# Kernel optimization log

Hardware: AMD Instinct MI355X
Metric: run time of the kernel (lower is better)

The kernel has to match this reference:

```python
import jax, jax.numpy as jnp
import numpy as np

N = 100000
E = 3200000
IN_CH, HID, OUT = 256, 64, 32


def setup_inputs() -> dict:
    key = jax.random.key(0)
    ks = jax.random.split(key, 8)
    x = jax.random.normal(ks[0], (N, IN_CH), dtype=jnp.float32)
    edge_index = jax.random.randint(ks[1], (2, E), 0, N, dtype=jnp.int64)
    # Glorot-ish init for weights, zeros for biases (PyG GCNConv: lin has no bias; conv bias added post-aggregation)
    W1 = jax.random.normal(ks[2], (IN_CH, HID), dtype=jnp.float32) / np.sqrt(IN_CH)
    b1 = jnp.zeros((HID,), dtype=jnp.float32)
    W2 = jax.random.normal(ks[3], (HID, OUT), dtype=jnp.float32) / np.sqrt(HID)
    b2 = jnp.zeros((OUT,), dtype=jnp.float32)
    Wc = jax.random.normal(ks[4], (OUT, 1), dtype=jnp.float32) / np.sqrt(OUT)
    bc = jnp.zeros((1,), dtype=jnp.float32)
    return {"x": x, "edge_index": edge_index, "W1": W1, "b1": b1,
            "W2": W2, "b2": b2, "Wc": Wc, "bc": bc}


def _gcn_norm(edge_index, num_nodes):
    # Add self-loops (PyG default), compute symmetric normalization D^{-1/2} A D^{-1/2}
    loops = jnp.arange(num_nodes, dtype=edge_index.dtype)
    row = jnp.concatenate([edge_index[0], loops])  # source
    col = jnp.concatenate([edge_index[1], loops])  # target (aggregation index)
    ones = jnp.ones(row.shape[0], dtype=jnp.float32)
    deg = jax.ops.segment_sum(ones, col, num_segments=num_nodes)
    dis = jnp.where(deg > 0, jax.lax.rsqrt(jnp.maximum(deg, 1e-12)), 0.0)
    norm = dis[row] * dis[col]  # [E+N]
    return row, col, norm


def _gcn_conv(x, W, b, row, col, norm, num_nodes):
    h = x @ W                                   # [N, F_out] dense transform first
    msg = h[row] * norm[:, None]                # gather + scale per edge
    agg = jax.ops.segment_sum(msg, col, num_segments=num_nodes)
    return agg + b


def reference(x, edge_index, W1, b1, W2, b2, Wc, bc):
    num_nodes = x.shape[0]
    row, col, norm = _gcn_norm(edge_index, num_nodes)
    h = jax.nn.elu(_gcn_conv(x, W1, b1, row, col, norm, num_nodes))
    h = jax.nn.elu(_gcn_conv(h, W2, b2, row, col, norm, num_nodes))
    return (h @ Wc + bc)[:, 0]                  # squeeze(1) -> [N]
```

## Files before the change

### kernel.cpp

```cpp
#include <hip/hip_runtime.h>
#include <hip/hip_fp16.h>
#include <math.h>

#define N_NODES 100000
#define N_EDGES 3200000
#define IN_CH   256
#define HID     64
#define OUTC    32
#define NB      ((N_NODES + 255) / 256)
#define NBUCK   ((N_NODES + 127) / 128)
#define CHUNK   4096
#define EPT     16
#define CAP     4608

static constexpr size_t align256(size_t x) { return (x + 255) & ~(size_t)255; }
static constexpr size_t OFF_DEG  = 0;
static constexpr size_t OFF_PTR  = OFF_DEG  + align256((size_t)N_NODES * 4);
static constexpr size_t OFF_BSUM = OFF_PTR  + align256((size_t)N_NODES * 4);
static constexpr size_t OFF_GCUR = OFF_BSUM + align256(512 * 4);
static constexpr size_t OFF_DIS  = OFF_GCUR + align256((size_t)NBUCK * 4);
static constexpr size_t OFF_SRC  = OFF_DIS  + align256((size_t)N_NODES * 4);
static constexpr size_t OFF_PART = OFF_SRC  + align256((size_t)N_EDGES * 4);
static constexpr size_t OFF_S1   = OFF_PART;
static constexpr size_t OFF_S2   = OFF_PART + align256((size_t)NBUCK * CAP * 4);

__global__ __launch_bounds__(256) void bucket_init(int* __restrict__ gcur) {
    int b = blockIdx.x * 256 + threadIdx.x;
    if (b < NBUCK) gcur[b] = b * CAP;
}

__global__ __launch_bounds__(256) void partition_edges(const int* __restrict__ row,
                                                       const int* __restrict__ col,
                                                       int* __restrict__ gcur,
                                                       int* __restrict__ part) {
    __shared__ int lhist[NBUCK];
    __shared__ int lbase[NBUCK];
    const int t  = threadIdx.x;
    const int e0 = blockIdx.x * CHUNK;
    for (int i = t; i < NBUCK; i += 256) lhist[i] = 0;
    __syncthreads();

    int pk[EPT], br[EPT];
#pragma unroll
    for (int i = 0; i < EPT; ++i) {
        int e = e0 + i * 256 + t;
        if (e < N_EDGES) {
            int d = col[e];
            int b = d >> 7;
            int r = atomicAdd(&lhist[b], 1);
            pk[i] = row[e] | ((d & 127) << 17);
            br[i] = b | (r << 10);
        } else {
            br[i] = -1;
        }
    }
    __syncthreads();

    const int off = (int)((blockIdx.x * 131u) % NBUCK);
    for (int i = t; i < NBUCK; i += 256) {
        int bb = i + off;
        if (bb >= NBUCK) bb -= NBUCK;
        int c = lhist[bb];
        lbase[bb] = (c > 0) ? atomicAdd(&gcur[bb], c) : 0;
    }
    __syncthreads();

#pragma unroll
    for (int i = 0; i < EPT; ++i) {
        if (br[i] >= 0) {
            int b = br[i] & 1023;
            int r = br[i] >> 10;
            part[lbase[b] + r] = pk[i];
        }
    }
}

__global__ __launch_bounds__(256) void bucket_hist(const int* __restrict__ gcur,
                                                   const int* __restrict__ part,
                                                   int* __restrict__ deg,
                                                   float* __restrict__ dis) {
    __shared__ int lh[128];
    const int b = blockIdx.x;
    const int t = threadIdx.x;
    if (t < 128) lh[t] = 0;
    __syncthreads();
    const int cnt = gcur[b] - b * CAP;
    for (int i = t; i < cnt; i += 256)
        atomicAdd(&lh[part[(size_t)b * CAP + i] >> 17], 1);
    __syncthreads();
    int v = b * 128 + t;
    if (t < 128 && v < N_NODES) {
        int d = lh[t];
        deg[v] = d;
        dis[v] = rsqrtf((float)d + 1.0f);
    }
}

__global__ __launch_bounds__(256) void scan_block_sums(const int* __restrict__ deg,
                                                       int* __restrict__ bsum) {
    __shared__ int buf[256];
    unsigned i = blockIdx.x * 256u + threadIdx.x;
    int v = (i < N_NODES) ? deg[i] : 0;
    buf[threadIdx.x] = v;
    __syncthreads();
    for (int off = 128; off > 0; off >>= 1) {
        if (threadIdx.x < (unsigned)off) buf[threadIdx.x] += buf[threadIdx.x + off];
        __syncthreads();
    }
    if (threadIdx.x == 0) bsum[blockIdx.x] = buf[0];
}

__global__ __launch_bounds__(512) void scan_bsum(int* __restrict__ bsum) {
    __shared__ int buf[512];
    int t = threadIdx.x;
    int v = (t < NB) ? bsum[t] : 0;
    buf[t] = v;
    __syncthreads();
    for (int off = 1; off < 512; off <<= 1) {
        int add = (t >= off) ? buf[t - off] : 0;
        __syncthreads();
        buf[t] += add;
        __syncthreads();
    }
    if (t < NB) bsum[t] = buf[t] - v;
}

__global__ __launch_bounds__(256) void scan_block_scan(const int* __restrict__ deg,
                                                       const int* __restrict__ bsum,
                                                       int* __restrict__ ptr) {
    __shared__ int buf[256];
    unsigned i = blockIdx.x * 256u + threadIdx.x;
    int v = (i < N_NODES) ? deg[i] : 0;
    buf[threadIdx.x] = v;
    __syncthreads();
    for (int off = 1; off < 256; off <<= 1) {
        int add = (threadIdx.x >= (unsigned)off) ? buf[threadIdx.x - off] : 0;
        __syncthreads();
        buf[threadIdx.x] += add;
        __syncthreads();
    }
    if (i < N_NODES) ptr[i] = bsum[blockIdx.x] + buf[threadIdx.x] - v;
}

__global__ __launch_bounds__(256) void bucket_fill(const int* __restrict__ gcur,
                                                   const int* __restrict__ part,
                                                   const int* __restrict__ ptr,
                                                   int* __restrict__ srcs) {
    __shared__ int lcur[128];
    const int b = blockIdx.x;
    const int t = threadIdx.x;
    if (t < 128) lcur[t] = 0;
    __syncthreads();
    const int cnt = gcur[b] - b * CAP;
    for (int i = t; i < cnt; i += 256) {
        int p    = part[(size_t)b * CAP + i];
        int dlow = p >> 17;
        int src  = p & 0x1FFFF;
        int r    = atomicAdd(&lcur[dlow], 1);
        srcs[ptr[b * 128 + dlow] + r] = src;
    }
}

__global__ __launch_bounds__(256) void gemm1(const float* __restrict__ x,
                                             const float* __restrict__ W1,
                                             const float* __restrict__ dis,
                                             __half* __restrict__ s1h) {
    __shared__ float wlds[64 * HID];
    __shared__ float xlds[64 * 68];

    const int t  = threadIdx.x;
    const int tx = t & 15;
    const int ty = t >> 4;
    const int row0 = blockIdx.x * 64;

    float acc[4][4] = {{0.f}};

    for (int kt = 0; kt < IN_CH / 64; ++kt) {
        {
            const float4* w4 = (const float4*)(W1 + (size_t)kt * 64 * HID);
            float4* l4 = (float4*)wlds;
#pragma unroll
            for (int i = 0; i < 4; ++i) l4[i * 256 + t] = w4[i * 256 + t];
        }
        {
#pragma unroll
            for (int i = 0; i < 4; ++i) {
                int L  = i * 256 + t;
                int rl = L >> 4;
                int k4 = L & 15;
                int rg = row0 + rl;
                float4 v;
                if (rg < N_NODES) v = ((const float4*)x)[(size_t)rg * 64 + kt * 16 + k4];
                else              v = make_float4(0.f, 0.f, 0.f, 0.f);
                *(float4*)(&xlds[rl * 68 + k4 * 4]) = v;
            }
        }
        __syncthreads();

        const float4* wl4 = (const float4*)wlds;
#pragma unroll 4
        for (int k4 = 0; k4 < 16; ++k4) {
            float4 xv[4];
#pragma unroll
            for (int i = 0; i < 4; ++i)
                xv[i] = *(const float4*)(&xlds[(ty * 4 + i) * 68 + k4 * 4]);
#pragma unroll
            for (int kk = 0; kk < 4; ++kk) {
                float4 bv = wl4[(k4 * 4 + kk) * 16 + tx];
#pragma unroll
                for (int i = 0; i < 4; ++i) {
                    const float* xf = (const float*)&xv[i];
                    float a = xf[kk];
                    acc[i][0] += a * bv.x;
                    acc[i][1] += a * bv.y;
                    acc[i][2] += a * bv.z;
                    acc[i][3] += a * bv.w;
                }
            }
        }
        __syncthreads();
    }

#pragma unroll
    for (int i = 0; i < 4; ++i) {
        int rr = row0 + ty * 4 + i;
        if (rr < N_NODES) {
            float d = dis[rr];
            __half2 p0 = __floats2half2_rn(acc[i][0] * d, acc[i][1] * d);
            __half2 p1 = __floats2half2_rn(acc[i][2] * d, acc[i][3] * d);
            __half2* dst = (__half2*)(s1h + (size_t)rr * HID + tx * 4);
            dst[0] = p0;
            dst[1] = p1;
        }
    }
}

__global__ __launch_bounds__(256) void gather1(const __half* __restrict__ s1h,
                                               const int* __restrict__ ptr,
                                               const int* __restrict__ srcs,
                                               const float* __restrict__ dis,
                                               const float* __restrict__ b1,
                                               const float* __restrict__ W2,
                                               __half* __restrict__ s2h) {
    __shared__ float w2lds[HID * OUTC];
    __shared__ float hbuf[4][HID];

    const int t = threadIdx.x;
    {
        float4* l4 = (float4*)w2lds;
        const float4* s4 = (const float4*)W2;
        l4[t] = s4[t];
        l4[256 + t] = s4[256 + t];
    }
    __syncthreads();

    const int j = t & 63;
    const int w = t >> 6;
    const int l = j & 31;
    const int h = j >> 5;
    const int v = __builtin_amdgcn_readfirstlane(blockIdx.x * 4 + w);
    const __half2* s12 = (const __half2*)s1h;

    float2 acc;
    {
        float2 self = __half22float2(s12[(size_t)v * 32 + l]);
        acc = (h == 0) ? self : make_float2(0.f, 0.f);
    }
    const int beg = ptr[v];
    const int end = (v + 1 < N_NODES) ? ptr[v + 1] : N_EDGES;
    int k = beg;
    for (; k + 8 <= end; k += 8) {
        int u0 = srcs[k],     u1 = srcs[k + 1], u2 = srcs[k + 2], u3 = srcs[k + 3];
        int u4 = srcs[k + 4], u5 = srcs[k + 5], u6 = srcs[k + 6], u7 = srcs[k + 7];
        int a0 = (h == 0) ? u0 : u1;
        int a1 = (h == 0) ? u2 : u3;
        int a2 = (h == 0) ? u4 : u5;
        int a3 = (h == 0) ? u6 : u7;
        float2 g0 = __half22float2(s12[(size_t)a0 * 32 + l]);
        float2 g1 = __half22float2(s12[(size_t)a1 * 32 + l]);
        float2 g2 = __half22float2(s12[(size_t)a2 * 32 + l]);
        float2 g3 = __half22float2(s12[(size_t)a3 * 32 + l]);
        acc.x += (g0.x + g1.x) + (g2.x + g3.x);
        acc.y += (g0.y + g1.y) + (g2.y + g3.y);
    }
    for (; k + 2 <= end; k += 2) {
        int u0 = srcs[k], u1 = srcs[k + 1];
        int a = (h == 0) ? u0 : u1;
        float2 g = __half22float2(s12[(size_t)a * 32 + l]);
        acc.x += g.x;
        acc.y += g.y;
    }
    if (k < end && h == 0) {
        float2 g = __half22float2(s12[(size_t)srcs[k] * 32 + l]);
        acc.x += g.x;
        acc.y += g.y;
    }
    acc.x += __shfl_xor(acc.x, 32, 64);
    acc.y += __shfl_xor(acc.y, 32, 64);

    float dv = dis[v];
    float2 bb = *(const float2*)(b1 + 2 * l);
    float t0 = dv * acc.x + bb.x;
    float t1 = dv * acc.y + bb.y;
    float h0 = t0 > 0.f ? t0 : (expf(t0) - 1.f);
    float h1 = t1 > 0.f ? t1 : (expf(t1) - 1.f);
    if (h == 0) {
        hbuf[w][2 * l]     = h0;
        hbuf[w][2 * l + 1] = h1;
    }

    const int jo = j & 31;
    const int kb = (j >> 5) * 32;
    float p = 0.f;
#pragma unroll
    for (int kk = 0; kk < 32; ++kk)
        p += hbuf[w][kb + kk] * w2lds[(kb + kk) * OUTC + jo];
    p += __shfl_xor(p, 32, 64);
    if (j < 32) {
        s2h[(size_t)v * OUTC + jo] = __float2half(dv * p);
    }
}

__global__ __launch_bounds__(256) void gather2(const __half* __restrict__ s2h,
                                               const int* __restrict__ ptr,
                                               const int* __restrict__ srcs,
                                               const float* __restrict__ dis,
                                               const float* __restrict__ b2,
                                               const float* __restrict__ Wc,
                                               const float* __restrict__ bc,
                                               float* __restrict__ out) {
    const int j = threadIdx.x & 63;
    const int w = threadIdx.x >> 6;
    const int l = j & 15;
    const int q = j >> 4;
    const int v = __builtin_amdgcn_readfirstlane(blockIdx.x * 4 + w);
    const __half2* s22 = (const __half2*)s2h;

    float2 acc;
    {
        float2 self = __half22float2(s22[(size_t)v * 16 + l]);
        acc = (q == 0) ? self : make_float2(0.f, 0.f);
    }
    const int beg = ptr[v];
    const int end = (v + 1 < N_NODES) ? ptr[v + 1] : N_EDGES;
    int k = beg;
    for (; k + 8 <= end; k += 8) {
        int a0 = srcs[k + q];
        int a1 = srcs[k + 4 + q];
        float2 g0 = __half22float2(s22[(size_t)a0 * 16 + l]);
        float2 g1 = __half22float2(s22[(size_t)a1 * 16 + l]);
        acc.x += g0.x + g1.x;
        acc.y += g0.y + g1.y;
    }
    for (; k + 4 <= end; k += 4) {
        int a = srcs[k + q];
        float2 g = __half22float2(s22[(size_t)a * 16 + l]);
        acc.x += g.x;
        acc.y += g.y;
    }
    int rem = end - k;
    if (q < rem) {
        int a = srcs[k + q];
        float2 g = __half22float2(s22[(size_t)a * 16 + l]);
        acc.x += g.x;
        acc.y += g.y;
    }
    acc.x += __shfl_xor(acc.x, 16, 64);
    acc.x += __shfl_xor(acc.x, 32, 64);
    acc.y += __shfl_xor(acc.y, 16, 64);
    acc.y += __shfl_xor(acc.y, 32, 64);

    float dv = dis[v];
    float2 bb = *(const float2*)(b2 + 2 * l);
    float t0 = dv * acc.x + bb.x;
    float t1 = dv * acc.y + bb.y;
    float h0 = t0 > 0.f ? t0 : (expf(t0) - 1.f);
    float h1 = t1 > 0.f ? t1 : (expf(t1) - 1.f);
    float2 wc = *(const float2*)(Wc + 2 * l);
    float p = h0 * wc.x + h1 * wc.y;
#pragma unroll
    for (int off = 8; off > 0; off >>= 1) p += __shfl_xor(p, off, 64);
    if (j == 0) out[v] = p + bc[0];
}

extern "C" void kernel_launch(void* const* d_in, const int* in_sizes, int n_in,
                              void* d_out, int out_size, void* d_ws, size_t ws_size,
                              hipStream_t stream) {
    const float* x  = (const float*)d_in[0];
    const int*   ei = (const int*)d_in[1];
    const float* W1 = (const float*)d_in[2];
    const float* b1 = (const float*)d_in[3];
    const float* W2 = (const float*)d_in[4];
    const float* b2 = (const float*)d_in[5];
    const float* Wc = (const float*)d_in[6];
    const float* bc = (const float*)d_in[7];
    float* out = (float*)d_out;

    const int* row = ei;
    const int* col = ei + N_EDGES;

    char* ws = (char*)d_ws;
    int*    deg  = (int*)   (ws + OFF_DEG);
    int*    ptr  = (int*)   (ws + OFF_PTR);
    int*    bsum = (int*)   (ws + OFF_BSUM);
    int*    gcur = (int*)   (ws + OFF_GCUR);
    float*  dis  = (float*) (ws + OFF_DIS);
    int*    srcs = (int*)   (ws + OFF_SRC);
    int*    part = (int*)   (ws + OFF_PART);
    __half* s1h  = (__half*)(ws + OFF_S1);
    __half* s2h  = (__half*)(ws + OFF_S2);

    bucket_init    <<<(NBUCK + 255) / 256, 256, 0, stream>>>(gcur);
    partition_edges<<<(N_EDGES + CHUNK - 1) / CHUNK, 256, 0, stream>>>(row, col, gcur, part);
    bucket_hist    <<<NBUCK, 256, 0, stream>>>(gcur, part, deg, dis);
    scan_block_sums<<<NB, 256, 0, stream>>>(deg, bsum);
    scan_bsum      <<<1, 512, 0, stream>>>(bsum);
    scan_block_scan<<<NB, 256, 0, stream>>>(deg, bsum, ptr);
    bucket_fill    <<<NBUCK, 256, 0, stream>>>(gcur, part, ptr, srcs);

    gemm1  <<<(N_NODES + 63) / 64, 256, 0, stream>>>(x, W1, dis, s1h);
    gather1<<<N_NODES / 4, 256, 0, stream>>>(s1h, ptr, srcs, dis, b1, W2, s2h);
    gather2<<<N_NODES / 4, 256, 0, stream>>>(s2h, ptr, srcs, dis, b2, Wc, bc, out);
}
```

Measured before the change: 417.6 us.

## Replace global degree scan with per-bucket local CSR offsets and deepen gather unroll

Builds the CSR with begin/end pointers local to each bucket's fixed-capacity region, computed by an in-block prefix scan inside bucket_hist. This removes the three global scan kernels and their launches. The source array becomes padded to NBUCK*CAP entries, and bucket_fill caches its base offsets in LDS. The gather loops are also unrolled to 16 edges per iteration, which puts more loads in flight at the cost of more registers.

Measured after the change: 414.5 us. About the same (-0.7%).

```diff
diff --git a/kernel.cpp b/kernel.cpp
--- a/kernel.cpp
+++ b/kernel.cpp
@@ -7,20 +7,18 @@
 #define IN_CH   256
 #define HID     64
 #define OUTC    32
-#define NB      ((N_NODES + 255) / 256)
 #define NBUCK   ((N_NODES + 127) / 128)
 #define CHUNK   4096
 #define EPT     16
 #define CAP     4608
 
 static constexpr size_t align256(size_t x) { return (x + 255) & ~(size_t)255; }
-static constexpr size_t OFF_DEG  = 0;
-static constexpr size_t OFF_PTR  = OFF_DEG  + align256((size_t)N_NODES * 4);
-static constexpr size_t OFF_BSUM = OFF_PTR  + align256((size_t)N_NODES * 4);
-static constexpr size_t OFF_GCUR = OFF_BSUM + align256(512 * 4);
+static constexpr size_t OFF_PTRB = 0;
+static constexpr size_t OFF_PTRE = OFF_PTRB + align256((size_t)N_NODES * 4);
+static constexpr size_t OFF_GCUR = OFF_PTRE + align256((size_t)N_NODES * 4);
 static constexpr size_t OFF_DIS  = OFF_GCUR + align256((size_t)NBUCK * 4);
 static constexpr size_t OFF_SRC  = OFF_DIS  + align256((size_t)N_NODES * 4);
-static constexpr size_t OFF_PART = OFF_SRC  + align256((size_t)N_EDGES * 4);
+static constexpr size_t OFF_PART = OFF_SRC  + align256((size_t)NBUCK * CAP * 4);
 static constexpr size_t OFF_S1   = OFF_PART;
 static constexpr size_t OFF_S2   = OFF_PART + align256((size_t)NBUCK * CAP * 4);
 
@@ -77,9 +75,11 @@
 
 __global__ __launch_bounds__(256) void bucket_hist(const int* __restrict__ gcur,
                                                    const int* __restrict__ part,
-                                                   int* __restrict__ deg,
+                                                   int* __restrict__ ptrb,
+                                                   int* __restrict__ ptre,
                                                    float* __restrict__ dis) {
     __shared__ int lh[128];
+    __shared__ int ls[128];
     const int b = blockIdx.x;
     const int t = threadIdx.x;
     if (t < 128) lh[t] = 0;
@@ -88,68 +88,37 @@
     for (int i = t; i < cnt; i += 256)
         atomicAdd(&lh[part[(size_t)b * CAP + i] >> 17], 1);
     __syncthreads();
+    int val = (t < 128) ? lh[t] : 0;
+    if (t < 128) ls[t] = val;
+    __syncthreads();
+    for (int off = 1; off < 128; off <<= 1) {
+        int add = (t >= off && t < 128) ? ls[t - off] : 0;
+        __syncthreads();
+        if (t < 128) ls[t] += add;
+        __syncthreads();
+    }
     int v = b * 128 + t;
     if (t < 128 && v < N_NODES) {
-        int d = lh[t];
-        deg[v] = d;
-        dis[v] = rsqrtf((float)d + 1.0f);
-    }
-}
-
-__global__ __launch_bounds__(256) void scan_block_sums(const int* __restrict__ deg,
-                                                       int* __restrict__ bsum) {
-    __shared__ int buf[256];
-    unsigned i = blockIdx.x * 256u + threadIdx.x;
-    int v = (i < N_NODES) ? deg[i] : 0;
-    buf[threadIdx.x] = v;
-    __syncthreads();
-    for (int off = 128; off > 0; off >>= 1) {
-        if (threadIdx.x < (unsigned)off) buf[threadIdx.x] += buf[threadIdx.x + off];
-        __syncthreads();
-    }
-    if (threadIdx.x == 0) bsum[blockIdx.x] = buf[0];
-}
-
-__global__ __launch_bounds__(512) void scan_bsum(int* __restrict__ bsum) {
-    __shared__ int buf[512];
-    int t = threadIdx.x;
-    int v = (t < NB) ? bsum[t] : 0;
-    buf[t] = v;
-    __syncthreads();
-    for (int off = 1; off < 512; off <<= 1) {
-        int add = (t >= off) ? buf[t - off] : 0;
-        __syncthreads();
-        buf[t] += add;
-        __syncthreads();
-    }
-    if (t < NB) bsum[t] = buf[t] - v;
-}
-
-__global__ __launch_bounds__(256) void scan_block_scan(const int* __restrict__ deg,
-                                                       const int* __restrict__ bsum,
-                                                       int* __restrict__ ptr) {
-    __shared__ int buf[256];
-    unsigned i = blockIdx.x * 256u + threadIdx.x;
-    int v = (i < N_NODES) ? deg[i] : 0;
-    buf[threadIdx.x] = v;
-    __syncthreads();
-    for (int off = 1; off < 256; off <<= 1) {
-        int add = (threadIdx.x >= (unsigned)off) ? buf[threadIdx.x - off] : 0;
-        __syncthreads();
-        buf[threadIdx.x] += add;
-        __syncthreads();
-    }
-    if (i < N_NODES) ptr[i] = bsum[blockIdx.x] + buf[threadIdx.x] - v;
+        int excl = ls[t] - val;
+        ptrb[v] = b * CAP + excl;
+        ptre[v] = b * CAP + excl + val;
+        dis[v]  = rsqrtf((float)val + 1.0f);
+    }
 }
 
 __global__ __launch_bounds__(256) void bucket_fill(const int* __restrict__ gcur,
                                                    const int* __restrict__ part,
-                                                   const int* __restrict__ ptr,
+                                                   const int* __restrict__ ptrb,
                                                    int* __restrict__ srcs) {
     __shared__ int lcur[128];
+    __shared__ int lbase2[128];
     const int b = blockIdx.x;
     const int t = threadIdx.x;
-    if (t < 128) lcur[t] = 0;
+    if (t < 128) {
+        lcur[t] = 0;
+        int v = b * 128 + t;
+        lbase2[t] = (v < N_NODES) ? ptrb[v] : 0;
+    }
     __syncthreads();
     const int cnt = gcur[b] - b * CAP;
     for (int i = t; i < cnt; i += 256) {
@@ -157,7 +126,7 @@
         int dlow = p >> 17;
         int src  = p & 0x1FFFF;
         int r    = atomicAdd(&lcur[dlow], 1);
-        srcs[ptr[b * 128 + dlow] + r] = src;
+        srcs[lbase2[dlow] + r] = src;
     }
 }
 
@@ -236,7 +205,8 @@
 }
 
 __global__ __launch_bounds__(256) void gather1(const __half* __restrict__ s1h,
-                                               const int* __restrict__ ptr,
+                                               const int* __restrict__ ptrb,
+                                               const int* __restrict__ ptre,
                                                const int* __restrict__ srcs,
                                                const float* __restrict__ dis,
                                                const float* __restrict__ b1,
@@ -266,26 +236,31 @@
         float2 self = __half22float2(s12[(size_t)v * 32 + l]);
         acc = (h == 0) ? self : make_float2(0.f, 0.f);
     }
-    const int beg = ptr[v];
-    const int end = (v + 1 < N_NODES) ? ptr[v + 1] : N_EDGES;
+    const int beg = ptrb[v];
+    const int end = ptre[v];
     int k = beg;
-    for (; k + 8 <= end; k += 8) {
-        int u0 = srcs[k],     u1 = srcs[k + 1], u2 = srcs[k + 2], u3 = srcs[k + 3];
-        int u4 = srcs[k + 4], u5 = srcs[k + 5], u6 = srcs[k + 6], u7 = srcs[k + 7];
-        int a0 = (h == 0) ? u0 : u1;
-        int a1 = (h == 0) ? u2 : u3;
-        int a2 = (h == 0) ? u4 : u5;
-        int a3 = (h == 0) ? u6 : u7;
+    for (; k + 16 <= end; k += 16) {
+        int a0 = (h == 0) ? srcs[k]      : srcs[k + 1];
+        int a1 = (h == 0) ? srcs[k + 2]  : srcs[k + 3];
+        int a2 = (h == 0) ? srcs[k + 4]  : srcs[k + 5];
+        int a3 = (h == 0) ? srcs[k + 6]  : srcs[k + 7];
+        int a4 = (h == 0) ? srcs[k + 8]  : srcs[k + 9];
+        int a5 = (h == 0) ? srcs[k + 10] : srcs[k + 11];
+        int a6 = (h == 0) ? srcs[k + 12] : srcs[k + 13];
+        int a7 = (h == 0) ? srcs[k + 14] : srcs[k + 15];
         float2 g0 = __half22float2(s12[(size_t)a0 * 32 + l]);
         float2 g1 = __half22float2(s12[(size_t)a1 * 32 + l]);
         float2 g2 = __half22float2(s12[(size_t)a2 * 32 + l]);
         float2 g3 = __half22float2(s12[(size_t)a3 * 32 + l]);
-        acc.x += (g0.x + g1.x) + (g2.x + g3.x);
-        acc.y += (g0.y + g1.y) + (g2.y + g3.y);
+        float2 g4 = __half22float2(s12[(size_t)a4 * 32 + l]);
+        float2 g5 = __half22float2(s12[(size_t)a5 * 32 + l]);
+        float2 g6 = __half22float2(s12[(size_t)a6 * 32 + l]);
+        float2 g7 = __half22float2(s12[(size_t)a7 * 32 + l]);
+        acc.x += ((g0.x + g1.x) + (g2.x + g3.x)) + ((g4.x + g5.x) + (g6.x + g7.x));
+        acc.y += ((g0.y + g1.y) + (g2.y + g3.y)) + ((g4.y + g5.y) + (g6.y + g7.y));
     }
     for (; k + 2 <= end; k += 2) {
-        int u0 = srcs[k], u1 = srcs[k + 1];
-        int a = (h == 0) ? u0 : u1;
+        int a = (h == 0) ? srcs[k] : srcs[k + 1];
         float2 g = __half22float2(s12[(size_t)a * 32 + l]);
         acc.x += g.x;
         acc.y += g.y;
@@ -322,7 +297,8 @@
 }
 
 __global__ __launch_bounds__(256) void gather2(const __half* __restrict__ s2h,
-                                               const int* __restrict__ ptr,
+                                               const int* __restrict__ ptrb,
+                                               const int* __restrict__ ptre,
                                                const int* __restrict__ srcs,
                                                const float* __restrict__ dis,
                                                const float* __restrict__ b2,
@@ -341,16 +317,20 @@
         float2 self = __half22float2(s22[(size_t)v * 16 + l]);
         acc = (q == 0) ? self : make_float2(0.f, 0.f);
     }
-    const int beg = ptr[v];
-    const int end = (v + 1 < N_NODES) ? ptr[v + 1] : N_EDGES;
+    const int beg = ptrb[v];
+    const int end = ptre[v];
     int k = beg;
-    for (; k + 8 <= end; k += 8) {
+    for (; k + 16 <= end; k += 16) {
         int a0 = srcs[k + q];
         int a1 = srcs[k + 4 + q];
+        int a2 = srcs[k + 8 + q];
+        int a3 = srcs[k + 12 + q];
         float2 g0 = __half22float2(s22[(size_t)a0 * 16 + l]);
         float2 g1 = __half22float2(s22[(size_t)a1 * 16 + l]);
-        acc.x += g0.x + g1.x;
-        acc.y += g0.y + g1.y;
+        float2 g2 = __half22float2(s22[(size_t)a2 * 16 + l]);
+        float2 g3 = __half22float2(s22[(size_t)a3 * 16 + l]);
+        acc.x += (g0.x + g1.x) + (g2.x + g3.x);
+        acc.y += (g0.y + g1.y) + (g2.y + g3.y);
     }
     for (; k + 4 <= end; k += 4) {
         int a = srcs[k + q];
@@ -400,9 +380,8 @@
     const int* col = ei + N_EDGES;
 
     char* ws = (char*)d_ws;
-    int*    deg  = (int*)   (ws + OFF_DEG);
-    int*    ptr  = (int*)   (ws + OFF_PTR);
-    int*    bsum = (int*)   (ws + OFF_BSUM);
+    int*    ptrb = (int*)   (ws + OFF_PTRB);
+    int*    ptre = (int*)   (ws + OFF_PTRE);
     int*    gcur = (int*)   (ws + OFF_GCUR);
     float*  dis  = (float*) (ws + OFF_DIS);
     int*    srcs = (int*)   (ws + OFF_SRC);
@@ -412,13 +391,10 @@
 
     bucket_init    <<<(NBUCK + 255) / 256, 256, 0, stream>>>(gcur);
     partition_edges<<<(N_EDGES + CHUNK - 1) / CHUNK, 256, 0, stream>>>(row, col, gcur, part);
-    bucket_hist    <<<NBUCK, 256, 0, stream>>>(gcur, part, deg, dis);
-    scan_block_sums<<<NB, 256, 0, stream>>>(deg, bsum);
-    scan_bsum      <<<1, 512, 0, stream>>>(bsum);
-    scan_block_scan<<<NB, 256, 0, stream>>>(deg, bsum, ptr);
-    bucket_fill    <<<NBUCK, 256, 0, stream>>>(gcur, part, ptr, srcs);
+    bucket_hist    <<<NBUCK, 256, 0, stream>>>(gcur, part, ptrb, ptre, dis);
+    bucket_fill    <<<NBUCK, 256, 0, stream>>>(gcur, part, ptrb, srcs);
 
     gemm1  <<<(N_NODES + 63) / 64, 256, 0, stream>>>(x, W1, dis, s1h);
-    gather1<<<N_NODES / 4, 256, 0, stream>>>(s1h, ptr, srcs, dis, b1, W2, s2h);
-    gather2<<<N_NODES / 4, 256, 0, stream>>>(s2h, ptr, srcs, dis, b2, Wc, bc, out);
-}
+    gather1<<<N_NODES / 4, 256, 0, stream>>>(s1h, ptrb, ptre, srcs, dis, b1, W2, s2h);
+    gather2<<<N_NODES / 4, 256, 0, stream>>>(s2h, ptrb, ptre, srcs, dis, b2, Wc, bc, out);
+}
```
